# Kernel optimization log

Measured on AMD Instinct MI355X. Metric: run time of the kernel, lower is better.

The kernel has to match this reference:

```python
import jax, jax.numpy as jnp
import numpy as np

B = 2
NUM_EDGES = 50000          # line-graph nodes per sample
N = B * NUM_EDGES          # total nodes in batched graph
E = 400000                 # connectivity edges (before self-loops)
F_IN = 16                  # num_edge_features
TDIM = 64                  # time_embedding_dim
H, C = 4, 32               # heads, hidden_channels
HC = H * C                 # 128
NL_EXTRA = 3               # num_layers - 1
NCLASS = 2
THETA = 1.0
MAX_TIME = 1000.0
NEG_SLOPE = 0.2            # GATv2 leaky_relu slope (PyG default)

def _p(key, shape, s=0.05):
    return jax.random.normal(key, shape, dtype=jnp.float32) * s

def setup_inputs() -> dict:
    key = jax.random.key(0)
    ks = jax.random.split(key, 16)
    return {
        "x": jax.random.normal(ks[0], (N, F_IN), dtype=jnp.float32),
        "edge_index": jax.random.randint(ks[1], (2, E), 0, N, dtype=jnp.int32),
        "t": jax.random.randint(ks[2], (B,), 0, 1000, dtype=jnp.int32),
        "tW0": _p(ks[3], (TDIM, TDIM)), "tb0": jnp.zeros((TDIM,), jnp.float32),
        "tW1": _p(ks[4], (TDIM, TDIM)), "tb1": jnp.zeros((TDIM,), jnp.float32),
        "c0_Wl": _p(ks[5], (F_IN + TDIM, HC)), "c0_bl": jnp.zeros((HC,), jnp.float32),
        "c0_Wr": _p(ks[6], (F_IN + TDIM, HC)), "c0_br": jnp.zeros((HC,), jnp.float32),
        "c0_att": _p(ks[7], (H, C)), "c0_bias": jnp.zeros((HC,), jnp.float32),
        "r0_W": _p(ks[8], (F_IN + TDIM, HC)), "r0_b": jnp.zeros((HC,), jnp.float32),
        "cWl": _p(ks[9], (NL_EXTRA, HC, HC)),
        "cWr": _p(ks[10], (NL_EXTRA, HC, HC)),
        "catt": _p(ks[11], (NL_EXTRA, H, C)),
        "rW": _p(ks[12], (NL_EXTRA, HC, HC)), "rb": jnp.zeros((NL_EXTRA, HC), jnp.float32),
        "fdW": _p(ks[13], (HC, C)), "fdb": jnp.zeros((C,), jnp.float32),
        "acW": _p(ks[14], (C, NCLASS)), "acb": jnp.zeros((NCLASS,), jnp.float32),
    }

def _timestep_embedding(t):
    # Fairseq-style sinusoidal embedding, matches get_timestep_embedding
    ts = t.astype(jnp.float32) * (1000.0 / MAX_TIME)
    half = TDIM // 2
    freqs = jnp.exp(jnp.arange(half, dtype=jnp.float32) * (-jnp.log(10000.0) / (half - 1)))
    ang = ts[:, None] * freqs[None, :]
    return jnp.concatenate([jnp.sin(ang), jnp.cos(ang)], axis=1)  # [B, TDIM]

def _gatv2(x, Wl, bl, Wr, br, att, src, dst):
    # PyG GATv2Conv, concat=True, add_self_loops already in src/dst
    xl = x @ Wl
    xr = x @ Wr
    if bl is not None:
        xl = xl + bl
    if br is not None:
        xr = xr + br
    xl = xl.reshape(N, H, C)
    xr = xr.reshape(N, H, C)
    g = jax.nn.leaky_relu(xl[src] + xr[dst], NEG_SLOPE)          # [Etot, H, C]
    e = jnp.einsum('ehc,hc->eh', g, att)                          # [Etot, H]
    m = jax.ops.segment_max(e, dst, num_segments=N)
    ex = jnp.exp(e - m[dst])
    denom = jax.ops.segment_sum(ex, dst, num_segments=N)
    alpha = ex / denom[dst]
    out = jax.ops.segment_sum(alpha[:, :, None] * xl[src], dst, num_segments=N)
    return out.reshape(N, HC)

def reference(x, edge_index, t, tW0, tb0, tW1, tb1, c0_Wl, c0_bl, c0_Wr, c0_br,
              c0_att, c0_bias, r0_W, r0_b, cWl, cWr, catt, rW, rb,
              fdW, fdb, acW, acb):
    loops = jnp.arange(N, dtype=edge_index.dtype)
    src = jnp.concatenate([edge_index[0], loops])
    dst = jnp.concatenate([edge_index[1], loops])
    te = jax.nn.silu(_timestep_embedding(t) @ tW0 + tb0)
    te = jax.nn.silu(te @ tW1 + tb1)
    te = jnp.repeat(te, NUM_EDGES, axis=0)                        # repeat_interleave
    h = jnp.concatenate([x, te], axis=1)                          # [N, F_IN+TDIM]
    res = jax.nn.relu(h @ r0_W + r0_b)
    h = THETA * jax.nn.relu(_gatv2(h, c0_Wl, c0_bl, c0_Wr, c0_br, c0_att, src, dst) + c0_bias) + res
    for i in range(NL_EXTRA):
        res = jax.nn.relu(h @ rW[i] + rb[i])
        h = THETA * jax.nn.relu(_gatv2(h, cWl[i], None, cWr[i], None, catt[i], src, dst)) + res
    logits = (h @ fdW + fdb) @ acW + acb
    return logits.reshape(B, NUM_EDGES, NCLASS)
```

## Files before the change

kernel.cpp:

```cpp
#include <hip/hip_runtime.h>
#include <stdint.h>

#define NN 100000
#define EE 400000
#define NEDGE 50000
#define NBLK ((NN + 1023) / 1024)

typedef unsigned short u16;
typedef unsigned int u32;
typedef __attribute__((ext_vector_type(8))) __bf16 v8bf;
typedef __attribute__((ext_vector_type(4))) float v4f;

__device__ __forceinline__ float bf2f(u16 u) {
    return (float)__builtin_bit_cast(__bf16, u);
}
__device__ __forceinline__ u16 f2bf(float f) {
    __bf16 b = (__bf16)f;
    return __builtin_bit_cast(u16, b);
}
__device__ __forceinline__ void unpack8(const int4& v, float* f) {
    u32 a = (u32)v.x, b = (u32)v.y, c = (u32)v.z, d = (u32)v.w;
    f[0] = bf2f((u16)(a & 0xffff)); f[1] = bf2f((u16)(a >> 16));
    f[2] = bf2f((u16)(b & 0xffff)); f[3] = bf2f((u16)(b >> 16));
    f[4] = bf2f((u16)(c & 0xffff)); f[5] = bf2f((u16)(c >> 16));
    f[6] = bf2f((u16)(d & 0xffff)); f[7] = bf2f((u16)(d >> 16));
}

__global__ void k_time_embed(const int* __restrict__ t,
                             const float* __restrict__ tW0, const float* __restrict__ tb0,
                             const float* __restrict__ tW1, const float* __restrict__ tb1,
                             float* __restrict__ te_out) {
    __shared__ float emb[2][64];
    __shared__ float u1[2][64];
    int tid = threadIdx.x;
    int b = tid >> 6, j = tid & 63;
    float ts = (float)t[b];
    int jj = (j < 32) ? j : (j - 32);
    float fr = expf((float)jj * (-logf(10000.0f) / 31.0f));
    float ang = ts * fr;
    emb[b][j] = (j < 32) ? sinf(ang) : cosf(ang);
    __syncthreads();
    float s = tb0[j];
    for (int k = 0; k < 64; ++k) s += emb[b][k] * tW0[k * 64 + j];
    s = s / (1.0f + expf(-s));
    u1[b][j] = s;
    __syncthreads();
    float s2 = tb1[j];
    for (int k = 0; k < 64; ++k) s2 += u1[b][k] * tW1[k * 64 + j];
    s2 = s2 / (1.0f + expf(-s2));
    te_out[b * 64 + j] = s2;
}

__global__ __launch_bounds__(256) void k_build_h0(const float* __restrict__ x,
                                                  const float* __restrict__ te,
                                                  u16* __restrict__ h) {
    int idx = blockIdx.x * 256 + threadIdx.x;
    if (idx >= NN * 16) return;
    int node = idx >> 4;
    int c8 = (idx & 15) << 3;
    u32 w_[4];
    if (c8 < 80) {
        const float* sp = (c8 < 16) ? (x + node * 16 + c8)
                                    : (te + ((node >= NEDGE) ? 64 : 0) + (c8 - 16));
#pragma unroll
        for (int i = 0; i < 4; ++i)
            w_[i] = (u32)f2bf(sp[2 * i]) | ((u32)f2bf(sp[2 * i + 1]) << 16);
    } else {
        w_[0] = w_[1] = w_[2] = w_[3] = 0;
    }
    int4 outv = make_int4((int)w_[0], (int)w_[1], (int)w_[2], (int)w_[3]);
    *reinterpret_cast<int4*>(h + node * 128 + c8) = outv;
}

struct WPtrs { const float* p[12]; int K[12]; };

__global__ __launch_bounds__(256) void k_wperm(WPtrs wp, u16* __restrict__ Wp) {
    int idx = blockIdx.x * 256 + threadIdx.x;
    if (idx >= 12 * 16384) return;
    int m = idx >> 14;
    int r = idx & 16383;
    int j = r & 7;
    int lane = (r >> 3) & 63;
    int fragid = r >> 9;
    int nt = fragid & 3;
    int ks = (fragid >> 2) & 3;
    int wc = fragid >> 4;
    int k = ks * 32 + ((lane >> 4) << 3) + j;
    int col = wc * 64 + nt * 16 + (lane & 15);
    float f = (k < wp.K[m]) ? wp.p[m][k * 128 + col] : 0.0f;
    Wp[idx] = f2bf(f);
}

__global__ void k_wf(const float* __restrict__ fdW, const float* __restrict__ fdb,
                     const float* __restrict__ acW, const float* __restrict__ acb,
                     float* __restrict__ Wf, float* __restrict__ bfu) {
    int i = threadIdx.x;
    if (i < 256) {
        int r = i >> 1, c = i & 1;
        float s = 0.f;
        for (int k = 0; k < 32; ++k) s += fdW[r * 32 + k] * acW[k * 2 + c];
        Wf[i] = s;
    } else if (i < 258) {
        int c = i - 256;
        float s = acb[c];
        for (int k = 0; k < 32; ++k) s += fdb[k] * acW[k * 2 + c];
        bfu[c] = s;
    }
}

__global__ __launch_bounds__(256) void k_count(const int* __restrict__ ei, int* __restrict__ deg) {
    int e = blockIdx.x * 256 + threadIdx.x;
    if (e >= EE) return;
    atomicAdd(&deg[ei[EE + e]], 1);
}

__global__ __launch_bounds__(1024) void k_scan1(const int* __restrict__ deg,
                                                int* __restrict__ part, int* __restrict__ bsum) {
    __shared__ int wsum[16], woff[16];
    int tid = threadIdx.x, lane = tid & 63, wid = tid >> 6;
    int idx = blockIdx.x * 1024 + tid;
    int v = (idx < NN) ? deg[idx] : 0;
    int s = v;
#pragma unroll
    for (int off = 1; off < 64; off <<= 1) {
        int tv = __shfl_up(s, off);
        if (lane >= off) s += tv;
    }
    if (lane == 63) wsum[wid] = s;
    __syncthreads();
    if (wid == 0) {
        int ws_ = (lane < 16) ? wsum[lane] : 0;
        int t2 = ws_;
#pragma unroll
        for (int off = 1; off < 16; off <<= 1) {
            int tv = __shfl_up(t2, off);
            if (lane >= off) t2 += tv;
        }
        if (lane < 16) woff[lane] = t2 - ws_;
    }
    __syncthreads();
    int excl = woff[wid] + (s - v);
    if (idx < NN) part[idx] = excl;
    if (tid == 1023) bsum[blockIdx.x] = excl + v;
}

__global__ void k_scan2(const int* __restrict__ bsum, int* __restrict__ boff) {
    __shared__ int ws0;
    int tid = threadIdx.x;
    int lane = tid & 63, wid = tid >> 6;
    int v = (tid < NBLK) ? bsum[tid] : 0;
    int s = v;
#pragma unroll
    for (int off = 1; off < 64; off <<= 1) {
        int tv = __shfl_up(s, off);
        if (lane >= off) s += tv;
    }
    if (tid == 63) ws0 = s;
    __syncthreads();
    int excl = (s - v) + (wid ? ws0 : 0);
    if (tid < NBLK) boff[tid] = excl;
    if (tid == NBLK - 1) boff[NBLK] = excl + v;
}

__global__ __launch_bounds__(256) void k_scan3(const int* __restrict__ part, const int* __restrict__ boff,
                                               int* __restrict__ rowptr, int* __restrict__ cursor) {
    int idx = blockIdx.x * 256 + threadIdx.x;
    if (idx > NN) return;
    int v = (idx == NN) ? boff[NBLK] : (part[idx] + boff[idx >> 10]);
    rowptr[idx] = v;
    if (idx < NN) cursor[idx] = v;
}

__global__ __launch_bounds__(256) void k_fill(const int* __restrict__ ei,
                                              int* __restrict__ cursor, int* __restrict__ colv) {
    int e = blockIdx.x * 256 + threadIdx.x;
    if (e >= EE) return;
    int s = ei[e], d = ei[EE + e];
    int pos = atomicAdd(&cursor[d], 1);
    colv[pos] = s;
}

__global__ __launch_bounds__(256) void k_gemm3(const u16* __restrict__ A,
                                               const u16* __restrict__ Wp,
                                               const float* __restrict__ b0,
                                               const float* __restrict__ b1,
                                               const float* __restrict__ b2,
                                               u16* __restrict__ xl, u16* __restrict__ xr,
                                               u16* __restrict__ res) {
    __shared__ __align__(16) u16 lA[128 * 128];
    int tid = threadIdx.x;
    int lane = tid & 63, wid = tid >> 6;
    int wr = wid >> 1, wc = wid & 1;
    int row0 = blockIdx.x * 128;

#pragma unroll
    for (int i = 0; i < 8; ++i) {
        int chunk = tid + i * 256;
        int row = chunk >> 4;
        int cb = (chunk & 15) << 4;
        int sb = cb ^ ((row & 7) << 4);
        int grow = row0 + row;
        int4 v = make_int4(0, 0, 0, 0);
        if (grow < NN) v = *reinterpret_cast<const int4*>(A + grow * 128 + (cb >> 1));
        *reinterpret_cast<int4*>(reinterpret_cast<char*>(lA) + row * 256 + sb) = v;
    }
    __syncthreads();

    const float* bptr[3] = {b0, b1, b2};
    u16* optr[3] = {xl, xr, res};

#pragma unroll
    for (int o = 0; o < 3; ++o) {
        v8bf bF[4][4];
        {
            const u16* wb = Wp + o * 16384 + ((wc * 16) * 64 + lane) * 8;
#pragma unroll
            for (int ks = 0; ks < 4; ++ks)
#pragma unroll
                for (int nt = 0; nt < 4; ++nt)
                    bF[ks][nt] = *reinterpret_cast<const v8bf*>(wb + (ks * 4 + nt) * 512);
        }

        v4f acc[4][4];
        v4f vzero = {0.f, 0.f, 0.f, 0.f};
#pragma unroll
        for (int m = 0; m < 4; ++m)
#pragma unroll
            for (int nt = 0; nt < 4; ++nt) acc[m][nt] = vzero;

#pragma unroll
        for (int ks = 0; ks < 4; ++ks) {
            v8bf aF[4];
#pragma unroll
            for (int m = 0; m < 4; ++m) {
                int row = wr * 64 + m * 16 + (lane & 15);
                int kb = ks * 64 + ((lane >> 4) << 4);
                int sb = kb ^ ((row & 7) << 4);
                aF[m] = *reinterpret_cast<const v8bf*>(reinterpret_cast<const char*>(lA) + row * 256 + sb);
            }
#pragma unroll
            for (int m = 0; m < 4; ++m)
#pragma unroll
                for (int nt = 0; nt < 4; ++nt)
                    acc[m][nt] = __builtin_amdgcn_mfma_f32_16x16x32_bf16(bF[ks][nt], aF[m], acc[m][nt], 0, 0, 0);
        }

        const float* bp = bptr[o];
        u16* op = optr[o];
        int relu = (o == 2);
        float4 bv[4];
#pragma unroll
        for (int nt = 0; nt < 4; ++nt)
            bv[nt] = bp ? *reinterpret_cast<const float4*>(bp + wc * 64 + nt * 16 + ((lane >> 4) << 2))
                        : make_float4(0.f, 0.f, 0.f, 0.f);
#pragma unroll
        for (int m = 0; m < 4; ++m) {
            int arow = row0 + wr * 64 + m * 16 + (lane & 15);
            if (arow < NN) {
#pragma unroll
                for (int nt = 0; nt < 4; ++nt) {
                    float v0 = acc[m][nt][0] + bv[nt].x;
                    float v1 = acc[m][nt][1] + bv[nt].y;
                    float v2 = acc[m][nt][2] + bv[nt].z;
                    float v3 = acc[m][nt][3] + bv[nt].w;
                    if (relu) {
                        v0 = fmaxf(v0, 0.f); v1 = fmaxf(v1, 0.f);
                        v2 = fmaxf(v2, 0.f); v3 = fmaxf(v3, 0.f);
                    }
                    int2 pk;
                    pk.x = (int)((u32)f2bf(v0) | ((u32)f2bf(v1) << 16));
                    pk.y = (int)((u32)f2bf(v2) | ((u32)f2bf(v3) << 16));
                    *reinterpret_cast<int2*>(op + arow * 128 + wc * 64 + nt * 16 + ((lane >> 4) << 2)) = pk;
                }
            }
        }
    }
}

__global__ __launch_bounds__(256) void k_gat(const u16* __restrict__ xl, const u16* __restrict__ xr,
                                             const float* __restrict__ att,
                                             const int* __restrict__ rowptr, const int* __restrict__ colv,
                                             const u16* __restrict__ res, const float* __restrict__ bias,
                                             u16* __restrict__ h) {
    int tid = threadIdx.x;
    int lane = tid & 63;
    int grp = lane >> 4;
    int s = lane & 15;
    int dst = blockIdx.x * 16 + (tid >> 6) * 4 + grp;
    if (dst >= NN) return;
    int c0 = s * 8;
    float av[8];
    *reinterpret_cast<float4*>(av) = *reinterpret_cast<const float4*>(att + c0);
    *reinterpret_cast<float4*>(av + 4) = *reinterpret_cast<const float4*>(att + c0 + 4);
    int4 xrv = *reinterpret_cast<const int4*>(xr + dst * 128 + c0);
    float xrf[8];
    unpack8(xrv, xrf);
    float den = 0.f;
    float acc[8] = {0.f, 0.f, 0.f, 0.f, 0.f, 0.f, 0.f, 0.f};
    int rbeg = rowptr[dst], rend = rowptr[dst + 1];
    for (int base = rbeg - 1; base < rend; base += 4) {
        int nv = rend - base; if (nv > 4) nv = 4;
        int4 xsv[4];
#pragma unroll
        for (int i = 0; i < 4; ++i) {
            if (i < nv) {
                int r = base + i;
                int src = (r < rbeg) ? dst : colv[r];
                xsv[i] = *reinterpret_cast<const int4*>(xl + src * 128 + c0);
            }
        }
#pragma unroll
        for (int i = 0; i < 4; ++i) {
            if (i < nv) {
                float xs[8];
                unpack8(xsv[i], xs);
                float e = 0.f;
#pragma unroll
                for (int j = 0; j < 8; ++j) {
                    float gg = xs[j] + xrf[j];
                    gg = (gg > 0.f) ? gg : 0.2f * gg;
                    e = fmaf(gg, av[j], e);
                }
                e += __shfl_xor(e, 1, 4);
                e += __shfl_xor(e, 2, 4);
                float p = __expf(e);
                den += p;
#pragma unroll
                for (int j = 0; j < 8; ++j) acc[j] = fmaf(p, xs[j], acc[j]);
            }
        }
    }
    float inv = 1.0f / den;
    int4 rv = *reinterpret_cast<const int4*>(res + dst * 128 + c0);
    float rf[8];
    unpack8(rv, rf);
    float bvv[8] = {0.f, 0.f, 0.f, 0.f, 0.f, 0.f, 0.f, 0.f};
    if (bias) {
        *reinterpret_cast<float4*>(bvv) = *reinterpret_cast<const float4*>(bias + c0);
        *reinterpret_cast<float4*>(bvv + 4) = *reinterpret_cast<const float4*>(bias + c0 + 4);
    }
    u32 ow[4];
#pragma unroll
    for (int j2 = 0; j2 < 4; ++j2) {
        float o0 = fmaxf(acc[2 * j2] * inv + bvv[2 * j2], 0.f) + rf[2 * j2];
        float o1 = fmaxf(acc[2 * j2 + 1] * inv + bvv[2 * j2 + 1], 0.f) + rf[2 * j2 + 1];
        ow[j2] = (u32)f2bf(o0) | ((u32)f2bf(o1) << 16);
    }
    *reinterpret_cast<int4*>(h + dst * 128 + c0) = make_int4((int)ow[0], (int)ow[1], (int)ow[2], (int)ow[3]);
}

__global__ __launch_bounds__(256) void k_final(const u16* __restrict__ h,
                                               const float* __restrict__ Wf, const float* __restrict__ bfu,
                                               float* __restrict__ out) {
    int tid = threadIdx.x;
    int row = blockIdx.x * 16 + (tid >> 4);
    int s = tid & 15;
    if (row >= NN) return;
    int4 hv = *reinterpret_cast<const int4*>(h + row * 128 + s * 8);
    float hf[8];
    unpack8(hv, hf);
    float v0 = 0.f, v1 = 0.f;
#pragma unroll
    for (int j = 0; j < 8; ++j) {
        v0 = fmaf(hf[j], Wf[(s * 8 + j) * 2], v0);
        v1 = fmaf(hf[j], Wf[(s * 8 + j) * 2 + 1], v1);
    }
#pragma unroll
    for (int off = 1; off < 16; off <<= 1) {
        v0 += __shfl_xor(v0, off, 16);
        v1 += __shfl_xor(v1, off, 16);
    }
    if (s == 0) {
        float2 o = make_float2(v0 + bfu[0], v1 + bfu[1]);
        *reinterpret_cast<float2*>(out + row * 2) = o;
    }
}

extern "C" void kernel_launch(void* const* d_in, const int* in_sizes, int n_in,
                              void* d_out, int out_size, void* d_ws, size_t ws_size,
                              hipStream_t stream) {
    const float* x      = (const float*)d_in[0];
    const int*   ei     = (const int*)d_in[1];
    const int*   t      = (const int*)d_in[2];
    const float* tW0    = (const float*)d_in[3];
    const float* tb0    = (const float*)d_in[4];
    const float* tW1    = (const float*)d_in[5];
    const float* tb1    = (const float*)d_in[6];
    const float* c0_Wl  = (const float*)d_in[7];
    const float* c0_bl  = (const float*)d_in[8];
    const float* c0_Wr  = (const float*)d_in[9];
    const float* c0_br  = (const float*)d_in[10];
    const float* c0_att = (const float*)d_in[11];
    const float* c0_bias= (const float*)d_in[12];
    const float* r0_W   = (const float*)d_in[13];
    const float* r0_b   = (const float*)d_in[14];
    const float* cWl    = (const float*)d_in[15];
    const float* cWr    = (const float*)d_in[16];
    const float* catt   = (const float*)d_in[17];
    const float* rW     = (const float*)d_in[18];
    const float* rb     = (const float*)d_in[19];
    const float* fdW    = (const float*)d_in[20];
    const float* fdb    = (const float*)d_in[21];
    const float* acW    = (const float*)d_in[22];
    const float* acb    = (const float*)d_in[23];
    (void)in_sizes; (void)n_in; (void)out_size; (void)ws_size;

    char* w = (char*)d_ws;
    const size_t HB = (size_t)NN * 128 * 2;
    float* te   = (float*)w;
    u16* h      = (u16*)(w + 4096);
    u16* xl     = (u16*)(w + 4096 + HB);
    u16* xr     = (u16*)(w + 4096 + 2 * HB);
    u16* res    = (u16*)(w + 4096 + 3 * HB);
    char* p     = w + 4096 + 4 * HB;
    int* deg    = (int*)(p);
    int* rowptr = (int*)(p + (1 << 19));
    int* cursor = (int*)(p + 2 * (1 << 19));
    int* colv   = (int*)(p + 3 * (1 << 19));
    int* part   = (int*)(p + 5 * (1 << 19));
    int* bsum   = (int*)(p + 6 * (1 << 19));
    int* boff   = (int*)(p + 6 * (1 << 19) + 4096);
    u16* Wp     = (u16*)(p + 7 * (1 << 19));
    float* Wf   = (float*)(p + 8 * (1 << 19));
    float* bfu  = (float*)(p + 8 * (1 << 19) + 2048);

    WPtrs wp;
    wp.p[0] = c0_Wl; wp.p[1] = c0_Wr; wp.p[2] = r0_W;
    wp.K[0] = 80;    wp.K[1] = 80;    wp.K[2] = 80;
    for (int i = 0; i < 3; ++i) {
        wp.p[3 + 3 * i] = cWl + i * 16384;
        wp.p[4 + 3 * i] = cWr + i * 16384;
        wp.p[5 + 3 * i] = rW + i * 16384;
        wp.K[3 + 3 * i] = 128; wp.K[4 + 3 * i] = 128; wp.K[5 + 3 * i] = 128;
    }
    k_wperm<<<768, 256, 0, stream>>>(wp, Wp);
    k_wf<<<1, 320, 0, stream>>>(fdW, fdb, acW, acb, Wf, bfu);

    k_time_embed<<<1, 128, 0, stream>>>(t, tW0, tb0, tW1, tb1, te);
    k_build_h0<<<(NN * 16 + 255) / 256, 256, 0, stream>>>(x, te, h);
    hipMemsetAsync(deg, 0, NN * sizeof(int), stream);
    k_count<<<(EE + 255) / 256, 256, 0, stream>>>(ei, deg);
    k_scan1<<<NBLK, 1024, 0, stream>>>(deg, part, bsum);
    k_scan2<<<1, 128, 0, stream>>>(bsum, boff);
    k_scan3<<<(NN + 256) / 256, 256, 0, stream>>>(part, boff, rowptr, cursor);
    k_fill<<<(EE + 255) / 256, 256, 0, stream>>>(ei, cursor, colv);

    const int GB = (NN + 127) / 128;
    const int GG = (NN + 15) / 16;
    k_gemm3<<<GB, 256, 0, stream>>>(h, Wp, c0_bl, c0_br, r0_b, xl, xr, res);
    k_gat<<<GG, 256, 0, stream>>>(xl, xr, c0_att, rowptr, colv, res, c0_bias, h);
    for (int i = 0; i < 3; ++i) {
        k_gemm3<<<GB, 256, 0, stream>>>(h, Wp + (3 + 3 * i) * 16384, nullptr, nullptr, rb + i * 128, xl, xr, res);
        k_gat<<<GG, 256, 0, stream>>>(xl, xr, catt + i * 128, rowptr, colv, res, nullptr, h);
    }
    k_final<<<GG, 256, 0, stream>>>(h, Wf, bfu, (float*)d_out);
}
```

Baseline: 488.1 us.

## Merge setup kernels, fuse final projection into last GAT, stage GEMM stores via LDS

Folds weight permutation, time embedding, final-weight folding and degree zeroing into one setup kernel, merges h0 construction with degree counting, and merges scan2 into scan3. The final linear projection is fused into the last GAT layer so the last h write and the separate k_final pass are skipped. GEMM epilogue now writes through a shared-memory transpose so global stores are full 16-byte rows. This cuts launch count and memory traffic, but the merged h0/count kernel reads te written by the previous launch (fine), and the LDS staging adds syncthreads and shared memory that may lower GEMM occupancy.

```diff
diff --git a/kernel.cpp b/kernel.cpp
--- a/kernel.cpp
+++ b/kernel.cpp
@@ -26,92 +26,101 @@
     f[6] = bf2f((u16)(d & 0xffff)); f[7] = bf2f((u16)(d >> 16));
 }
 
-__global__ void k_time_embed(const int* __restrict__ t,
-                             const float* __restrict__ tW0, const float* __restrict__ tb0,
-                             const float* __restrict__ tW1, const float* __restrict__ tb1,
-                             float* __restrict__ te_out) {
+struct WPtrs { const float* p[12]; int K[12]; };
+
+__global__ __launch_bounds__(256) void k_setup(WPtrs wp, u16* __restrict__ Wp,
+        const int* __restrict__ t,
+        const float* __restrict__ tW0, const float* __restrict__ tb0,
+        const float* __restrict__ tW1, const float* __restrict__ tb1,
+        float* __restrict__ te_out,
+        const float* __restrict__ fdW, const float* __restrict__ fdb,
+        const float* __restrict__ acW, const float* __restrict__ acb,
+        float* __restrict__ Wf, float* __restrict__ bfu,
+        int* __restrict__ deg) {
     __shared__ float emb[2][64];
     __shared__ float u1[2][64];
-    int tid = threadIdx.x;
-    int b = tid >> 6, j = tid & 63;
-    float ts = (float)t[b];
-    int jj = (j < 32) ? j : (j - 32);
-    float fr = expf((float)jj * (-logf(10000.0f) / 31.0f));
-    float ang = ts * fr;
-    emb[b][j] = (j < 32) ? sinf(ang) : cosf(ang);
-    __syncthreads();
-    float s = tb0[j];
-    for (int k = 0; k < 64; ++k) s += emb[b][k] * tW0[k * 64 + j];
-    s = s / (1.0f + expf(-s));
-    u1[b][j] = s;
-    __syncthreads();
-    float s2 = tb1[j];
-    for (int k = 0; k < 64; ++k) s2 += u1[b][k] * tW1[k * 64 + j];
-    s2 = s2 / (1.0f + expf(-s2));
-    te_out[b * 64 + j] = s2;
-}
-
-__global__ __launch_bounds__(256) void k_build_h0(const float* __restrict__ x,
-                                                  const float* __restrict__ te,
-                                                  u16* __restrict__ h) {
-    int idx = blockIdx.x * 256 + threadIdx.x;
-    if (idx >= NN * 16) return;
-    int node = idx >> 4;
-    int c8 = (idx & 15) << 3;
-    u32 w_[4];
-    if (c8 < 80) {
-        const float* sp = (c8 < 16) ? (x + node * 16 + c8)
-                                    : (te + ((node >= NEDGE) ? 64 : 0) + (c8 - 16));
-#pragma unroll
-        for (int i = 0; i < 4; ++i)
-            w_[i] = (u32)f2bf(sp[2 * i]) | ((u32)f2bf(sp[2 * i + 1]) << 16);
-    } else {
-        w_[0] = w_[1] = w_[2] = w_[3] = 0;
-    }
-    int4 outv = make_int4((int)w_[0], (int)w_[1], (int)w_[2], (int)w_[3]);
-    *reinterpret_cast<int4*>(h + node * 128 + c8) = outv;
-}
-
-struct WPtrs { const float* p[12]; int K[12]; };
-
-__global__ __launch_bounds__(256) void k_wperm(WPtrs wp, u16* __restrict__ Wp) {
-    int idx = blockIdx.x * 256 + threadIdx.x;
-    if (idx >= 12 * 16384) return;
-    int m = idx >> 14;
-    int r = idx & 16383;
-    int j = r & 7;
-    int lane = (r >> 3) & 63;
-    int fragid = r >> 9;
-    int nt = fragid & 3;
-    int ks = (fragid >> 2) & 3;
-    int wc = fragid >> 4;
-    int k = ks * 32 + ((lane >> 4) << 3) + j;
-    int col = wc * 64 + nt * 16 + (lane & 15);
-    float f = (k < wp.K[m]) ? wp.p[m][k * 128 + col] : 0.0f;
-    Wp[idx] = f2bf(f);
-}
-
-__global__ void k_wf(const float* __restrict__ fdW, const float* __restrict__ fdb,
-                     const float* __restrict__ acW, const float* __restrict__ acb,
-                     float* __restrict__ Wf, float* __restrict__ bfu) {
-    int i = threadIdx.x;
-    if (i < 256) {
-        int r = i >> 1, c = i & 1;
+    int b = blockIdx.x, tid = threadIdx.x;
+    if (b < 768) {
+        int idx = b * 256 + tid;
+        int m = idx >> 14;
+        int r = idx & 16383;
+        int j = r & 7;
+        int lane = (r >> 3) & 63;
+        int fragid = r >> 9;
+        int nt = fragid & 3;
+        int ks = (fragid >> 2) & 3;
+        int wc = fragid >> 4;
+        int k = ks * 32 + ((lane >> 4) << 3) + j;
+        int col = wc * 64 + nt * 16 + (lane & 15);
+        float f = (k < wp.K[m]) ? wp.p[m][k * 128 + col] : 0.0f;
+        Wp[idx] = f2bf(f);
+    } else if (b == 768) {
+        if (tid < 128) {
+            int bb = tid >> 6, j = tid & 63;
+            float ts = (float)t[bb];
+            int jj = (j < 32) ? j : (j - 32);
+            float fr = expf((float)jj * (-logf(10000.0f) / 31.0f));
+            float ang = ts * fr;
+            emb[bb][j] = (j < 32) ? sinf(ang) : cosf(ang);
+        }
+        __syncthreads();
+        if (tid < 128) {
+            int bb = tid >> 6, j = tid & 63;
+            float s = tb0[j];
+            for (int k = 0; k < 64; ++k) s += emb[bb][k] * tW0[k * 64 + j];
+            s = s / (1.0f + expf(-s));
+            u1[bb][j] = s;
+        }
+        __syncthreads();
+        if (tid < 128) {
+            int bb = tid >> 6, j = tid & 63;
+            float s2 = tb1[j];
+            for (int k = 0; k < 64; ++k) s2 += u1[bb][k] * tW1[k * 64 + j];
+            s2 = s2 / (1.0f + expf(-s2));
+            te_out[bb * 64 + j] = s2;
+        }
+    } else if (b == 769) {
+        int r = tid >> 1, c = tid & 1;
         float s = 0.f;
         for (int k = 0; k < 32; ++k) s += fdW[r * 32 + k] * acW[k * 2 + c];
-        Wf[i] = s;
-    } else if (i < 258) {
-        int c = i - 256;
-        float s = acb[c];
-        for (int k = 0; k < 32; ++k) s += fdb[k] * acW[k * 2 + c];
-        bfu[c] = s;
-    }
-}
-
-__global__ __launch_bounds__(256) void k_count(const int* __restrict__ ei, int* __restrict__ deg) {
-    int e = blockIdx.x * 256 + threadIdx.x;
-    if (e >= EE) return;
-    atomicAdd(&deg[ei[EE + e]], 1);
+        Wf[tid] = s;
+        if (tid < 2) {
+            float s2 = acb[tid];
+            for (int k = 0; k < 32; ++k) s2 += fdb[k] * acW[k * 2 + tid];
+            bfu[tid] = s2;
+        }
+    } else {
+        int i = (b - 770) * 256 + tid;
+        if (i < NN) deg[i] = 0;
+    }
+}
+
+__global__ __launch_bounds__(256) void k_h0count(const float* __restrict__ x,
+                                                 const float* __restrict__ te,
+                                                 u16* __restrict__ h,
+                                                 const int* __restrict__ ei,
+                                                 int* __restrict__ deg) {
+    int b = blockIdx.x, tid = threadIdx.x;
+    if (b < 6250) {
+        int idx = b * 256 + tid;
+        int node = idx >> 4;
+        int c8 = (idx & 15) << 3;
+        u32 w_[4];
+        if (c8 < 80) {
+            const float* sp = (c8 < 16) ? (x + node * 16 + c8)
+                                        : (te + ((node >= NEDGE) ? 64 : 0) + (c8 - 16));
+#pragma unroll
+            for (int i = 0; i < 4; ++i)
+                w_[i] = (u32)f2bf(sp[2 * i]) | ((u32)f2bf(sp[2 * i + 1]) << 16);
+        } else {
+            w_[0] = w_[1] = w_[2] = w_[3] = 0;
+        }
+        int4 outv = make_int4((int)w_[0], (int)w_[1], (int)w_[2], (int)w_[3]);
+        *reinterpret_cast<int4*>(h + node * 128 + c8) = outv;
+    } else {
+        int e = (b - 6250) * 256 + tid;
+        if (e < EE) atomicAdd(&deg[ei[EE + e]], 1);
+    }
 }
 
 __global__ __launch_bounds__(1024) void k_scan1(const int* __restrict__ deg,
@@ -144,31 +153,34 @@
     if (tid == 1023) bsum[blockIdx.x] = excl + v;
 }
 
-__global__ void k_scan2(const int* __restrict__ bsum, int* __restrict__ boff) {
-    __shared__ int ws0;
+__global__ __launch_bounds__(256) void k_scan3(const int* __restrict__ part, const int* __restrict__ bsum,
+                                               int* __restrict__ rowptr, int* __restrict__ cursor) {
+    __shared__ int pre[NBLK + 1];
+    __shared__ int sh_ws0;
     int tid = threadIdx.x;
     int lane = tid & 63, wid = tid >> 6;
-    int v = (tid < NBLK) ? bsum[tid] : 0;
-    int s = v;
-#pragma unroll
-    for (int off = 1; off < 64; off <<= 1) {
-        int tv = __shfl_up(s, off);
-        if (lane >= off) s += tv;
-    }
-    if (tid == 63) ws0 = s;
+    int v = 0, s = 0;
+    if (tid < 128) {
+        v = (tid < NBLK) ? bsum[tid] : 0;
+        s = v;
+#pragma unroll
+        for (int off = 1; off < 64; off <<= 1) {
+            int tv = __shfl_up(s, off);
+            if (lane >= off) s += tv;
+        }
+        if (tid == 63) sh_ws0 = s;
+    }
     __syncthreads();
-    int excl = (s - v) + (wid ? ws0 : 0);
-    if (tid < NBLK) boff[tid] = excl;
-    if (tid == NBLK - 1) boff[NBLK] = excl + v;
-}
-
-__global__ __launch_bounds__(256) void k_scan3(const int* __restrict__ part, const int* __restrict__ boff,
-                                               int* __restrict__ rowptr, int* __restrict__ cursor) {
-    int idx = blockIdx.x * 256 + threadIdx.x;
+    if (tid < 128) {
+        int excl = (s - v) + (wid ? sh_ws0 : 0);
+        if (tid <= NBLK) pre[tid] = excl;
+    }
+    __syncthreads();
+    int idx = blockIdx.x * 256 + tid;
     if (idx > NN) return;
-    int v = (idx == NN) ? boff[NBLK] : (part[idx] + boff[idx >> 10]);
-    rowptr[idx] = v;
-    if (idx < NN) cursor[idx] = v;
+    int val = (idx == NN) ? pre[NBLK] : (part[idx] + pre[idx >> 10]);
+    rowptr[idx] = val;
+    if (idx < NN) cursor[idx] = val;
 }
 
 __global__ __launch_bounds__(256) void k_fill(const int* __restrict__ ei,
@@ -188,6 +200,7 @@
                                                u16* __restrict__ xl, u16* __restrict__ xr,
                                                u16* __restrict__ res) {
     __shared__ __align__(16) u16 lA[128 * 128];
+    __shared__ __align__(16) u16 lT[4][32][72];
     int tid = threadIdx.x;
     int lane = tid & 63, wid = tid >> 6;
     int wr = wid >> 1, wc = wid & 1;
@@ -253,10 +266,14 @@
         for (int nt = 0; nt < 4; ++nt)
             bv[nt] = bp ? *reinterpret_cast<const float4*>(bp + wc * 64 + nt * 16 + ((lane >> 4) << 2))
                         : make_float4(0.f, 0.f, 0.f, 0.f);
-#pragma unroll
-        for (int m = 0; m < 4; ++m) {
-            int arow = row0 + wr * 64 + m * 16 + (lane & 15);
-            if (arow < NN) {
+
+#pragma unroll
+        for (int p = 0; p < 2; ++p) {
+#pragma unroll
+            for (int mm = 0; mm < 2; ++mm) {
+                int m = p * 2 + mm;
+                int rl = mm * 16 + (lane & 15);
+                int cl = (lane >> 4) << 2;
 #pragma unroll
                 for (int nt = 0; nt < 4; ++nt) {
                     float v0 = acc[m][nt][0] + bv[nt].x;
@@ -270,9 +287,19 @@
                     int2 pk;
                     pk.x = (int)((u32)f2bf(v0) | ((u32)f2bf(v1) << 16));
                     pk.y = (int)((u32)f2bf(v2) | ((u32)f2bf(v3) << 16));
-                    *reinterpret_cast<int2*>(op + arow * 128 + wc * 64 + nt * 16 + ((lane >> 4) << 2)) = pk;
+                    *reinterpret_cast<int2*>(&lT[wid][rl][nt * 16 + cl]) = pk;
                 }
             }
+            __syncthreads();
+#pragma unroll
+            for (int i = 0; i < 4; ++i) {
+                int rl2 = i * 8 + (lane >> 3);
+                int4 v = *reinterpret_cast<const int4*>(&lT[wid][rl2][(lane & 7) * 8]);
+                int grow = row0 + wr * 64 + p * 32 + rl2;
+                if (grow < NN)
+                    *reinterpret_cast<int4*>(op + grow * 128 + wc * 64 + (lane & 7) * 8) = v;
+            }
+            __syncthreads();
         }
     }
 }
@@ -281,7 +308,9 @@
                                              const float* __restrict__ att,
                                              const int* __restrict__ rowptr, const int* __restrict__ colv,
                                              const u16* __restrict__ res, const float* __restrict__ bias,
-                                             u16* __restrict__ h) {
+                                             u16* __restrict__ h,
+                                             const float* __restrict__ Wf, const float* __restrict__ bfu,
+                                             float* __restrict__ out) {
     int tid = threadIdx.x;
     int lane = tid & 63;
     int grp = lane >> 4;
@@ -339,40 +368,32 @@
         *reinterpret_cast<float4*>(bvv) = *reinterpret_cast<const float4*>(bias + c0);
         *reinterpret_cast<float4*>(bvv + 4) = *reinterpret_cast<const float4*>(bias + c0 + 4);
     }
-    u32 ow[4];
-#pragma unroll
-    for (int j2 = 0; j2 < 4; ++j2) {
-        float o0 = fmaxf(acc[2 * j2] * inv + bvv[2 * j2], 0.f) + rf[2 * j2];
-        float o1 = fmaxf(acc[2 * j2 + 1] * inv + bvv[2 * j2 + 1], 0.f) + rf[2 * j2 + 1];
-        ow[j2] = (u32)f2bf(o0) | ((u32)f2bf(o1) << 16);
-    }
-    *reinterpret_cast<int4*>(h + dst * 128 + c0) = make_int4((int)ow[0], (int)ow[1], (int)ow[2], (int)ow[3]);
-}
-
-__global__ __launch_bounds__(256) void k_final(const u16* __restrict__ h,
-                                               const float* __restrict__ Wf, const float* __restrict__ bfu,
-                                               float* __restrict__ out) {
-    int tid = threadIdx.x;
-    int row = blockIdx.x * 16 + (tid >> 4);
-    int s = tid & 15;
-    if (row >= NN) return;
-    int4 hv = *reinterpret_cast<const int4*>(h + row * 128 + s * 8);
-    float hf[8];
-    unpack8(hv, hf);
-    float v0 = 0.f, v1 = 0.f;
-#pragma unroll
-    for (int j = 0; j < 8; ++j) {
-        v0 = fmaf(hf[j], Wf[(s * 8 + j) * 2], v0);
-        v1 = fmaf(hf[j], Wf[(s * 8 + j) * 2 + 1], v1);
-    }
-#pragma unroll
-    for (int off = 1; off < 16; off <<= 1) {
-        v0 += __shfl_xor(v0, off, 16);
-        v1 += __shfl_xor(v1, off, 16);
-    }
-    if (s == 0) {
-        float2 o = make_float2(v0 + bfu[0], v1 + bfu[1]);
-        *reinterpret_cast<float2*>(out + row * 2) = o;
+    float of[8];
+#pragma unroll
+    for (int j = 0; j < 8; ++j)
+        of[j] = fmaxf(acc[j] * inv + bvv[j], 0.f) + rf[j];
+    if (out) {
+        float v0 = 0.f, v1 = 0.f;
+#pragma unroll
+        for (int j = 0; j < 8; ++j) {
+            v0 = fmaf(of[j], Wf[(c0 + j) * 2], v0);
+            v1 = fmaf(of[j], Wf[(c0 + j) * 2 + 1], v1);
+        }
+#pragma unroll
+        for (int off = 1; off < 16; off <<= 1) {
+            v0 += __shfl_xor(v0, off, 16);
+            v1 += __shfl_xor(v1, off, 16);
+        }
+        if (s == 0) {
+            float2 o = make_float2(v0 + bfu[0], v1 + bfu[1]);
+            *reinterpret_cast<float2*>(out + dst * 2) = o;
+        }
+    } else {
+        u32 ow[4];
+#pragma unroll
+        for (int j2 = 0; j2 < 4; ++j2)
+            ow[j2] = (u32)f2bf(of[2 * j2]) | ((u32)f2bf(of[2 * j2 + 1]) << 16);
+        *reinterpret_cast<int4*>(h + dst * 128 + c0) = make_int4((int)ow[0], (int)ow[1], (int)ow[2], (int)ow[3]);
     }
 }
 
@@ -419,7 +440,6 @@
     int* colv   = (int*)(p + 3 * (1 << 19));
     int* part   = (int*)(p + 5 * (1 << 19));
     int* bsum   = (int*)(p + 6 * (1 << 19));
-    int* boff   = (int*)(p + 6 * (1 << 19) + 4096);
     u16* Wp     = (u16*)(p + 7 * (1 << 19));
     float* Wf   = (float*)(p + 8 * (1 << 19));
     float* bfu  = (float*)(p + 8 * (1 << 19) + 2048);
@@ -433,25 +453,22 @@
         wp.p[5 + 3 * i] = rW + i * 16384;
         wp.K[3 + 3 * i] = 128; wp.K[4 + 3 * i] = 128; wp.K[5 + 3 * i] = 128;
     }
-    k_wperm<<<768, 256, 0, stream>>>(wp, Wp);
-    k_wf<<<1, 320, 0, stream>>>(fdW, fdb, acW, acb, Wf, bfu);
-
-    k_time_embed<<<1, 128, 0, stream>>>(t, tW0, tb0, tW1, tb1, te);
-    k_build_h0<<<(NN * 16 + 255) / 256, 256, 0, stream>>>(x, te, h);
-    hipMemsetAsync(deg, 0, NN * sizeof(int), stream);
-    k_count<<<(EE + 255) / 256, 256, 0, stream>>>(ei, deg);
+
+    k_setup<<<770 + 391, 256, 0, stream>>>(wp, Wp, t, tW0, tb0, tW1, tb1, te,
+                                           fdW, fdb, acW, acb, Wf, bfu, deg);
+    k_h0count<<<6250 + 1563, 256, 0, stream>>>(x, te, h, ei, deg);
     k_scan1<<<NBLK, 1024, 0, stream>>>(deg, part, bsum);
-    k_scan2<<<1, 128, 0, stream>>>(bsum, boff);
-    k_scan3<<<(NN + 256) / 256, 256, 0, stream>>>(part, boff, rowptr, cursor);
+    k_scan3<<<(NN + 256) / 256, 256, 0, stream>>>(part, bsum, rowptr, cursor);
     k_fill<<<(EE + 255) / 256, 256, 0, stream>>>(ei, cursor, colv);
 
     const int GB = (NN + 127) / 128;
     const int GG = (NN + 15) / 16;
     k_gemm3<<<GB, 256, 0, stream>>>(h, Wp, c0_bl, c0_br, r0_b, xl, xr, res);
-    k_gat<<<GG, 256, 0, stream>>>(xl, xr, c0_att, rowptr, colv, res, c0_bias, h);
+    k_gat<<<GG, 256, 0, stream>>>(xl, xr, c0_att, rowptr, colv, res, c0_bias, h,
+                                  nullptr, nullptr, nullptr);
     for (int i = 0; i < 3; ++i) {
         k_gemm3<<<GB, 256, 0, stream>>>(h, Wp + (3 + 3 * i) * 16384, nullptr, nullptr, rb + i * 128, xl, xr, res);
-        k_gat<<<GG, 256, 0, stream>>>(xl, xr, catt + i * 128, rowptr, colv, res, nullptr, h);
-    }
-    k_final<<<GG, 256, 0, stream>>>(h, Wf, bfu, (float*)d_out);
-}
+        k_gat<<<GG, 256, 0, stream>>>(xl, xr, catt + i * 128, rowptr, colv, res, nullptr, h,
+                                      Wf, bfu, (i == 2) ? (float*)d_out : nullptr);
+    }
+}
```

New measurement: 433.8 us. 1.13x faster.
